# Kernel optimization log

Measured on AMD Instinct MI355X. Metric: run time of the kernel, lower is better.

## Reference

```python
import jax, jax.numpy as jnp
import numpy as np

N_USER = 100000
N_ITEM = 150000
N = N_USER + N_ITEM
D = 64            # latdim
NNZ = 1250000     # sparse adjacency nnz
BATCH = 16384     # node_ids batch
NUM_GNN_LAYERS = 2
GD = 16           # gate_dim (mamba d_model)
DSTATE = 8
DCONV = 4
EXPAND = 2
DINNER = GD * EXPAND  # 32
DTRANK = 1            # ceil(GD/16)
TEMP = 0.8            # gate_temp


def setup_inputs() -> dict:
    key = jax.random.key(0)
    ks = jax.random.split(key, 20)
    f32 = jnp.float32
    inp = {}
    inp["user_embedding"] = jax.random.normal(ks[0], (N_USER, D), f32) * 0.02
    inp["item_embedding"] = jax.random.normal(ks[1], (N_ITEM, D), f32) * 0.02
    inp["edge_row"] = jax.random.randint(ks[2], (NNZ,), 0, N, dtype=jnp.int32)
    inp["edge_col"] = jax.random.randint(ks[3], (NNZ,), 0, N, dtype=jnp.int32)
    inp["edge_val"] = jax.random.uniform(ks[4], (NNZ,), f32) * 0.1
    inp["node_ids"] = jax.random.randint(ks[5], (BATCH,), 0, N, dtype=jnp.int32)
    # gate params (torch Linear weight layout: [out, in])
    inp["down_w"] = jax.random.normal(ks[6], (GD, D), f32) * 0.02
    inp["in_proj_w"] = jax.random.normal(ks[7], (2 * DINNER, GD), f32) * 0.05
    inp["conv_w"] = jax.random.normal(ks[8], (DINNER, DCONV), f32) * 0.1
    inp["conv_b"] = jnp.zeros((DINNER,), f32)
    inp["x_proj_w"] = jax.random.normal(ks[9], (DTRANK + 2 * DSTATE, DINNER), f32) * 0.05
    inp["dt_proj_w"] = jax.random.normal(ks[10], (DINNER, DTRANK), f32) * 0.1
    inp["dt_proj_b"] = jax.random.normal(ks[11], (DINNER,), f32) * 0.1
    inp["A_log"] = jnp.log(jnp.broadcast_to(jnp.arange(1, DSTATE + 1, dtype=f32), (DINNER, DSTATE)))
    inp["D_param"] = jnp.ones((DINNER,), f32)
    inp["out_proj_w"] = jax.random.normal(ks[12], (GD, DINNER), f32) * 0.05
    inp["ln_g"] = jnp.ones((GD,), f32)
    inp["ln_b"] = jnp.zeros((GD,), f32)
    inp["to_logit_w"] = jax.random.normal(ks[13], (1, GD), f32) * 0.02
    inp["to_logit_b"] = jnp.zeros((1,), f32)
    return inp


def _mamba(g, in_proj_w, conv_w, conv_b, x_proj_w, dt_proj_w, dt_proj_b, A_log, D_param, out_proj_w):
    # g: [B, L, GD] -- standard Mamba block (selective scan)
    Bsz, L, _ = g.shape
    xz = g @ in_proj_w.T                     # [B,L,2*DINNER]
    x, z = jnp.split(xz, 2, axis=-1)         # each [B,L,DINNER]
    # causal depthwise conv1d along L (padding = DCONV-1, truncated to L)
    xp = jnp.pad(x, ((0, 0), (DCONV - 1, 0), (0, 0)))
    xconv = sum(xp[:, k:k + L, :] * conv_w[:, k] for k in range(DCONV)) + conv_b
    x = jax.nn.silu(xconv)
    dbc = x @ x_proj_w.T                     # [B,L,DTRANK+2*DSTATE]
    dt = dbc[..., :DTRANK]
    Bm = dbc[..., DTRANK:DTRANK + DSTATE]
    Cm = dbc[..., DTRANK + DSTATE:]
    dt = jax.nn.softplus(dt @ dt_proj_w.T + dt_proj_b)   # [B,L,DINNER]
    A = -jnp.exp(A_log)                                   # [DINNER,DSTATE]
    dA = jnp.exp(dt[..., None] * A)                       # [B,L,DINNER,DSTATE]
    dBx = dt[..., None] * Bm[:, :, None, :] * x[..., None]

    def step(h, ins):
        dA_t, dBx_t = ins
        h = dA_t * h + dBx_t
        return h, h

    h0 = jnp.zeros((Bsz, DINNER, DSTATE), x.dtype)
    _, hs = jax.lax.scan(step, h0, (jnp.swapaxes(dA, 0, 1), jnp.swapaxes(dBx, 0, 1)))
    hs = jnp.swapaxes(hs, 0, 1)                           # [B,L,DINNER,DSTATE]
    y = jnp.einsum('blds,bls->bld', hs, Cm) + D_param * x
    y = y * jax.nn.silu(z)
    return y @ out_proj_w.T                               # [B,L,GD]


def reference(user_embedding, item_embedding, edge_val, down_w, in_proj_w, conv_w,
              conv_b, x_proj_w, dt_proj_w, dt_proj_b, A_log, D_param, out_proj_w,
              ln_g, ln_b, to_logit_w, to_logit_b, edge_row, edge_col, node_ids):
    embeds = jnp.concatenate([user_embedding, item_embedding], axis=0)   # [N,D]
    seqs = [embeds[node_ids]]
    for _ in range(NUM_GNN_LAYERS):
        # sparse adjacency aggregation: out[r] += val * embeds[c]
        msg = edge_val[:, None] * embeds[edge_col]                       # [NNZ,D]
        embeds = jax.ops.segment_sum(msg, edge_row, num_segments=N)      # [N,D]
        # F.normalize(p=2, dim=1)
        nrm = jnp.linalg.norm(embeds, axis=1, keepdims=True)
        embeds = embeds / jnp.maximum(nrm, 1e-12)
        seqs.append(embeds[node_ids])
    seq = jnp.stack(seqs, axis=1)                                        # [B,L,D]

    # MambaDepthGating._compute_logits (deg_cond disabled)
    g = seq @ down_w.T                                                   # [B,L,GD]
    y = _mamba(g, in_proj_w, conv_w, conv_b, x_proj_w, dt_proj_w, dt_proj_b,
               A_log, D_param, out_proj_w)
    y = y + g
    mu = y.mean(-1, keepdims=True)
    var = y.var(-1, keepdims=True)
    y = (y - mu) / jnp.sqrt(var + 1e-12) * ln_g + ln_b                   # LN eps=1e-12
    logits = (y @ to_logit_w.T + to_logit_b)[..., 0]                     # [B,L]

    # fuse_from_logits, L=3 > 2 -> softmax path, perturbed=False
    w = jax.nn.softmax(logits / max(TEMP, 1e-6), axis=1)                 # [B,L]
    fused = jnp.sum(seq * w[..., None], axis=1)                          # [B,D]
    return fused
```

## Files before the change

kernel.cpp:

```cpp
#include <hip/hip_runtime.h>
#include <math.h>

#define N_USER 100000
#define N_ITEM 150000
#define NTOT   250000
#define D64    64
#define NNZ    1250000
#define BATCH  16384
#define GD     16
#define DSTATE 8
#define DCONV  4
#define DINNER 32
#define LSEQ   3
#define NBLK1  ((NTOT + 1023) >> 10)

__global__ void zero4_kernel(int4* __restrict__ p, int n4) {
    int i = blockIdx.x * blockDim.x + threadIdx.x;
    if (i < n4) p[i] = make_int4(0, 0, 0, 0);
}

__global__ void mark_nids_kernel(const int* __restrict__ nids,
                                 unsigned char* __restrict__ nidf,
                                 unsigned char* __restrict__ needf) {
    int b = blockIdx.x * 256 + threadIdx.x;
    if (b < BATCH) { int r = nids[b]; nidf[r] = 1; needf[r] = 1; }
}

__global__ void mark_need_kernel(const int* __restrict__ erow,
                                 const int* __restrict__ ecol,
                                 const unsigned char* __restrict__ nidf,
                                 unsigned char* __restrict__ needf) {
    int e = blockIdx.x * 256 + threadIdx.x;
    if (e < NNZ && nidf[erow[e]]) needf[ecol[e]] = 1;
}

__global__ void hist_slot_kernel(const int* __restrict__ erow,
                                 const unsigned char* __restrict__ needf,
                                 int* __restrict__ cnt, int* __restrict__ slot) {
    int e = blockIdx.x * 256 + threadIdx.x;
    if (e >= NNZ) return;
    int r = erow[e];
    if (needf[r]) slot[e] = atomicAdd(&cnt[r], 1);
}

__global__ __launch_bounds__(256) void scan1_kernel(const int* __restrict__ cnt,
                                                    int* __restrict__ offs,
                                                    int* __restrict__ bsum) {
    __shared__ int lds[256];
    int t = threadIdx.x;
    int base = (blockIdx.x << 10) + (t << 2);
    int d0 = (base + 0 < NTOT) ? cnt[base + 0] : 0;
    int d1 = (base + 1 < NTOT) ? cnt[base + 1] : 0;
    int d2 = (base + 2 < NTOT) ? cnt[base + 2] : 0;
    int d3 = (base + 3 < NTOT) ? cnt[base + 3] : 0;
    int s = d0 + d1 + d2 + d3;
    lds[t] = s;
    __syncthreads();
    for (int off = 1; off < 256; off <<= 1) {
        int v = (t >= off) ? lds[t - off] : 0;
        __syncthreads();
        lds[t] += v;
        __syncthreads();
    }
    int excl = lds[t] - s;
    if (base + 0 < NTOT) offs[base + 0] = excl;
    if (base + 1 < NTOT) offs[base + 1] = excl + d0;
    if (base + 2 < NTOT) offs[base + 2] = excl + d0 + d1;
    if (base + 3 < NTOT) offs[base + 3] = excl + d0 + d1 + d2;
    if (t == 255) bsum[blockIdx.x] = lds[255];
}

__global__ __launch_bounds__(256) void scan2_kernel(int* __restrict__ bsum) {
    __shared__ int lds[256];
    int t = threadIdx.x;
    int v0 = (t < NBLK1) ? bsum[t] : 0;
    lds[t] = v0;
    __syncthreads();
    for (int off = 1; off < 256; off <<= 1) {
        int v = (t >= off) ? lds[t - off] : 0;
        __syncthreads();
        lds[t] += v;
        __syncthreads();
    }
    if (t < NBLK1) bsum[t] = lds[t] - v0;
}

__global__ void scan3_kernel(int* __restrict__ offs, const int* __restrict__ bsum,
                             const int* __restrict__ cnt) {
    int i = blockIdx.x * 256 + threadIdx.x;
    if (i >= NTOT) return;
    int v = offs[i] + bsum[i >> 10];
    offs[i] = v;
    if (i == NTOT - 1) offs[NTOT] = v + cnt[i];
}

__global__ void fill_kernel(const int* __restrict__ erow, const int* __restrict__ ecol,
                            const float* __restrict__ eval_, const int* __restrict__ offs,
                            const int* __restrict__ slot,
                            const unsigned char* __restrict__ needf,
                            int2* __restrict__ colval) {
    int e = blockIdx.x * 256 + threadIdx.x;
    if (e >= NNZ) return;
    int r = erow[e];
    if (!needf[r]) return;
    colval[offs[r] + slot[e]] = make_int2(ecol[e], __float_as_int(eval_[e]));
}

__global__ __launch_bounds__(256) void layer1_kernel(const float* __restrict__ user,
                                                     const float* __restrict__ item,
                                                     const unsigned char* __restrict__ needf,
                                                     const int*  __restrict__ offs,
                                                     const int2* __restrict__ colval,
                                                     float* __restrict__ dst) {
    const float4* user4 = (const float4*)user;
    const float4* item4 = (const float4*)item;

    int row    = (blockIdx.x << 4) + (threadIdx.x >> 4);
    int lane16 = threadIdx.x & 15;
    if (row >= NTOT) return;
    if (!needf[row]) return;
    int o0 = offs[row], o1 = offs[row + 1];

    float4 acc = make_float4(0.f, 0.f, 0.f, 0.f);
    int i = o0;
    for (; i + 2 <= o1; i += 2) {
        int2 cv0 = colval[i];
        int2 cv1 = colval[i + 1];
        const float4* s0 = (cv0.x < N_USER) ? user4 + (size_t)cv0.x * 16
                                            : item4 + (size_t)(cv0.x - N_USER) * 16;
        const float4* s1 = (cv1.x < N_USER) ? user4 + (size_t)cv1.x * 16
                                            : item4 + (size_t)(cv1.x - N_USER) * 16;
        float4 v0 = s0[lane16];
        float4 v1 = s1[lane16];
        float w0 = __int_as_float(cv0.y);
        float w1 = __int_as_float(cv1.y);
        acc.x = fmaf(w1, v1.x, fmaf(w0, v0.x, acc.x));
        acc.y = fmaf(w1, v1.y, fmaf(w0, v0.y, acc.y));
        acc.z = fmaf(w1, v1.z, fmaf(w0, v0.z, acc.z));
        acc.w = fmaf(w1, v1.w, fmaf(w0, v0.w, acc.w));
    }
    if (i < o1) {
        int2 cv = colval[i];
        const float4* s0 = (cv.x < N_USER) ? user4 + (size_t)cv.x * 16
                                           : item4 + (size_t)(cv.x - N_USER) * 16;
        float4 v = s0[lane16];
        float w = __int_as_float(cv.y);
        acc.x = fmaf(w, v.x, acc.x);
        acc.y = fmaf(w, v.y, acc.y);
        acc.z = fmaf(w, v.z, acc.z);
        acc.w = fmaf(w, v.w, acc.w);
    }

    float s = fmaf(acc.x, acc.x, fmaf(acc.y, acc.y, fmaf(acc.z, acc.z, acc.w * acc.w)));
    #pragma unroll
    for (int m = 8; m >= 1; m >>= 1) s += __shfl_xor(s, m, 64);
    float scale = 1.f / fmaxf(sqrtf(s), 1e-12f);
    float4 r;
    r.x = acc.x * scale; r.y = acc.y * scale; r.z = acc.z * scale; r.w = acc.w * scale;
    ((float4*)dst)[(size_t)row * 16 + lane16] = r;
}

__global__ __launch_bounds__(256) void layer2_kernel(const float* __restrict__ embA,
                                                     const int*  __restrict__ nids,
                                                     const int*  __restrict__ offs,
                                                     const int2* __restrict__ colval,
                                                     float* __restrict__ embBc) {
    const float4* src4 = (const float4*)embA;
    int idx    = (blockIdx.x << 4) + (threadIdx.x >> 4);
    int lane16 = threadIdx.x & 15;
    if (idx >= BATCH) return;
    int row = nids[idx];
    int o0 = offs[row], o1 = offs[row + 1];

    float4 acc = make_float4(0.f, 0.f, 0.f, 0.f);
    int i = o0;
    for (; i + 2 <= o1; i += 2) {
        int2 cv0 = colval[i];
        int2 cv1 = colval[i + 1];
        float4 v0 = src4[(size_t)cv0.x * 16 + lane16];
        float4 v1 = src4[(size_t)cv1.x * 16 + lane16];
        float w0 = __int_as_float(cv0.y);
        float w1 = __int_as_float(cv1.y);
        acc.x = fmaf(w1, v1.x, fmaf(w0, v0.x, acc.x));
        acc.y = fmaf(w1, v1.y, fmaf(w0, v0.y, acc.y));
        acc.z = fmaf(w1, v1.z, fmaf(w0, v0.z, acc.z));
        acc.w = fmaf(w1, v1.w, fmaf(w0, v0.w, acc.w));
    }
    if (i < o1) {
        int2 cv = colval[i];
        float4 v = src4[(size_t)cv.x * 16 + lane16];
        float w = __int_as_float(cv.y);
        acc.x = fmaf(w, v.x, acc.x);
        acc.y = fmaf(w, v.y, acc.y);
        acc.z = fmaf(w, v.z, acc.z);
        acc.w = fmaf(w, v.w, acc.w);
    }

    float s = fmaf(acc.x, acc.x, fmaf(acc.y, acc.y, fmaf(acc.z, acc.z, acc.w * acc.w)));
    #pragma unroll
    for (int m = 8; m >= 1; m >>= 1) s += __shfl_xor(s, m, 64);
    float scale = 1.f / fmaxf(sqrtf(s), 1e-12f);
    float4 r;
    r.x = acc.x * scale; r.y = acc.y * scale; r.z = acc.z * scale; r.w = acc.w * scale;
    ((float4*)embBc)[(size_t)idx * 16 + lane16] = r;
}

__global__ __launch_bounds__(64, 1) void final_kernel(
    const int*   __restrict__ nids,
    const float* __restrict__ user,      const float* __restrict__ item,
    const float* __restrict__ embA,      const float* __restrict__ embBc,
    const float* __restrict__ down_w,    const float* __restrict__ in_proj_w,
    const float* __restrict__ conv_w,    const float* __restrict__ conv_b,
    const float* __restrict__ x_proj_w,  const float* __restrict__ dt_proj_w,
    const float* __restrict__ dt_proj_b, const float* __restrict__ A_log,
    const float* __restrict__ D_param,   const float* __restrict__ out_proj_w,
    const float* __restrict__ ln_g,      const float* __restrict__ ln_b,
    const float* __restrict__ to_logit_w,const float* __restrict__ to_logit_b,
    float* __restrict__ out) {

    __shared__ float4 s_down4[GD * 16];
    __shared__ float4 s_ipx4[DINNER * 4];
    __shared__ float4 s_ipz4[DINNER * 4];
    __shared__ float  s_xpT[DINNER * 17];
    __shared__ float4 s_cw4[DINNER];
    __shared__ float  s_cb[DINNER];
    __shared__ float  s_dtw[DINNER], s_dtb[DINNER], s_Dp[DINNER];
    __shared__ float  s_A[DINNER * DSTATE];
    __shared__ float4 s_opT4[DINNER * 4];
    __shared__ float  s_lng[GD], s_lnb[GD], s_lw[GD];
    __shared__ float  s_lb;

    int t = threadIdx.x;
    {
        const float4* dw4 = (const float4*)down_w;
        for (int i = t; i < GD * 16; i += 64) s_down4[i] = dw4[i];
        const float4* ip4 = (const float4*)in_proj_w;
        for (int i = t; i < DINNER * 4; i += 64) { s_ipx4[i] = ip4[i]; s_ipz4[i] = ip4[DINNER * 4 + i]; }
        for (int i = t; i < DINNER * 17; i += 64) {
            int d = i / 17, r = i % 17;
            s_xpT[i] = x_proj_w[r * DINNER + d];
        }
        const float4* cw4 = (const float4*)conv_w;
        for (int i = t; i < DINNER; i += 64) {
            s_cw4[i] = cw4[i]; s_cb[i] = conv_b[i]; s_dtw[i] = dt_proj_w[i];
            s_dtb[i] = dt_proj_b[i]; s_Dp[i] = D_param[i];
        }
        for (int i = t; i < DINNER * DSTATE; i += 64) s_A[i] = -expf(A_log[i]);
        float* s_opT = (float*)s_opT4;
        for (int i = t; i < DINNER * GD; i += 64) {
            int d = i >> 4, j = i & 15;
            s_opT[i] = out_proj_w[j * DINNER + d];
        }
        if (t < GD) { s_lng[t] = ln_g[t]; s_lnb[t] = ln_b[t]; s_lw[t] = to_logit_w[t]; }
        if (t == 0) s_lb = to_logit_b[0];
    }
    __syncthreads();

    int b = blockIdx.x * 64 + t;
    int nid = nids[b];
    const float4* p0 = (const float4*)((nid < N_USER) ? user + (size_t)nid * D64
                                                      : item + (size_t)(nid - N_USER) * D64);
    const float4* p1 = (const float4*)(embA + (size_t)nid * D64);
    const float4* p2 = (const float4*)(embBc + (size_t)b * D64);

    float g[LSEQ][GD];
    #pragma unroll
    for (int l = 0; l < LSEQ; ++l)
        #pragma unroll
        for (int j = 0; j < GD; ++j) g[l][j] = 0.f;
    #pragma unroll
    for (int q = 0; q < 16; ++q) {
        float4 v0 = p0[q], v1 = p1[q], v2 = p2[q];
        #pragma unroll
        for (int j = 0; j < GD; ++j) {
            float4 w = s_down4[j * 16 + q];
            g[0][j] = fmaf(v0.x, w.x, fmaf(v0.y, w.y, fmaf(v0.z, w.z, fmaf(v0.w, w.w, g[0][j]))));
            g[1][j] = fmaf(v1.x, w.x, fmaf(v1.y, w.y, fmaf(v1.z, w.z, fmaf(v1.w, w.w, g[1][j]))));
            g[2][j] = fmaf(v2.x, w.x, fmaf(v2.y, w.y, fmaf(v2.z, w.z, fmaf(v2.w, w.w, g[2][j]))));
        }
    }

    #define COMPUTE_XS(d, xs0, xs1, xs2)                                          \
        float xs0, xs1, xs2;                                                      \
        {                                                                         \
            float xl0 = 0.f, xl1 = 0.f, xl2 = 0.f;                                \
            _Pragma("unroll")                                                     \
            for (int qq = 0; qq < 4; ++qq) {                                      \
                float4 w = s_ipx4[(d) * 4 + qq];                                  \
                xl0 = fmaf(g[0][4*qq+0], w.x, fmaf(g[0][4*qq+1], w.y,             \
                      fmaf(g[0][4*qq+2], w.z, fmaf(g[0][4*qq+3], w.w, xl0))));    \
                xl1 = fmaf(g[1][4*qq+0], w.x, fmaf(g[1][4*qq+1], w.y,             \
                      fmaf(g[1][4*qq+2], w.z, fmaf(g[1][4*qq+3], w.w, xl1))));    \
                xl2 = fmaf(g[2][4*qq+0], w.x, fmaf(g[2][4*qq+1], w.y,             \
                      fmaf(g[2][4*qq+2], w.z, fmaf(g[2][4*qq+3], w.w, xl2))));    \
            }                                                                     \
            float4 cw = s_cw4[d]; float cb = s_cb[d];                             \
            float a0 = fmaf(xl0, cw.w, cb);                                       \
            float a1 = fmaf(xl1, cw.w, fmaf(xl0, cw.z, cb));                      \
            float a2 = fmaf(xl2, cw.w, fmaf(xl1, cw.z, fmaf(xl0, cw.y, cb)));     \
            xs0 = a0 / (1.f + __expf(-a0));                                       \
            xs1 = a1 / (1.f + __expf(-a1));                                       \
            xs2 = a2 / (1.f + __expf(-a2));                                       \
        }

    float dtr[LSEQ] = {0.f, 0.f, 0.f};
    float Bm[LSEQ][DSTATE], Cm[LSEQ][DSTATE];
    #pragma unroll
    for (int l = 0; l < LSEQ; ++l)
        #pragma unroll
        for (int s = 0; s < DSTATE; ++s) { Bm[l][s] = 0.f; Cm[l][s] = 0.f; }

    for (int d = 0; d < DINNER; ++d) {
        COMPUTE_XS(d, xs0, xs1, xs2)
        const float* xt = s_xpT + d * 17;
        float w = xt[0];
        dtr[0] = fmaf(xs0, w, dtr[0]); dtr[1] = fmaf(xs1, w, dtr[1]); dtr[2] = fmaf(xs2, w, dtr[2]);
        #pragma unroll
        for (int s = 0; s < DSTATE; ++s) {
            float wb = xt[1 + s], wc = xt[9 + s];
            Bm[0][s] = fmaf(xs0, wb, Bm[0][s]); Bm[1][s] = fmaf(xs1, wb, Bm[1][s]); Bm[2][s] = fmaf(xs2, wb, Bm[2][s]);
            Cm[0][s] = fmaf(xs0, wc, Cm[0][s]); Cm[1][s] = fmaf(xs1, wc, Cm[1][s]); Cm[2][s] = fmaf(xs2, wc, Cm[2][s]);
        }
    }

    float o[LSEQ][GD];
    #pragma unroll
    for (int l = 0; l < LSEQ; ++l)
        #pragma unroll
        for (int j = 0; j < GD; ++j) o[l][j] = 0.f;

    for (int d = 0; d < DINNER; ++d) {
        COMPUTE_XS(d, ys0, ys1, ys2)
        float xsv[3] = {ys0, ys1, ys2};
        float As[DSTATE];
        #pragma unroll
        for (int s = 0; s < DSTATE; ++s) As[s] = s_A[d * DSTATE + s];
        float dtw = s_dtw[d], dtb = s_dtb[d], Dp = s_Dp[d];
        float h[DSTATE];
        #pragma unroll
        for (int s = 0; s < DSTATE; ++s) h[s] = 0.f;
        #pragma unroll
        for (int l = 0; l < LSEQ; ++l) {
            float pre = fmaf(dtr[l], dtw, dtb);
            float dt  = (pre > 20.f) ? pre : __logf(1.f + __expf(pre));
            float xv  = xsv[l];
            float dtx = dt * xv;
            float acc = 0.f;
            #pragma unroll
            for (int s = 0; s < DSTATE; ++s) {
                float dA = __expf(dt * As[s]);
                h[s] = fmaf(dA, h[s], dtx * Bm[l][s]);
                acc  = fmaf(h[s], Cm[l][s], acc);
            }
            float y = fmaf(Dp, xv, acc);
            float zv = 0.f;
            #pragma unroll
            for (int qq = 0; qq < 4; ++qq) {
                float4 w = s_ipz4[d * 4 + qq];
                zv = fmaf(g[l][4*qq+0], w.x, fmaf(g[l][4*qq+1], w.y,
                     fmaf(g[l][4*qq+2], w.z, fmaf(g[l][4*qq+3], w.w, zv))));
            }
            float ys = y * (zv / (1.f + __expf(-zv)));
            #pragma unroll
            for (int qq = 0; qq < 4; ++qq) {
                float4 w = s_opT4[d * 4 + qq];
                o[l][4*qq+0] = fmaf(ys, w.x, o[l][4*qq+0]);
                o[l][4*qq+1] = fmaf(ys, w.y, o[l][4*qq+1]);
                o[l][4*qq+2] = fmaf(ys, w.z, o[l][4*qq+2]);
                o[l][4*qq+3] = fmaf(ys, w.w, o[l][4*qq+3]);
            }
        }
    }

    float lg[LSEQ];
    #pragma unroll
    for (int l = 0; l < LSEQ; ++l) {
        float mu = 0.f;
        #pragma unroll
        for (int j = 0; j < GD; ++j) { o[l][j] += g[l][j]; mu += o[l][j]; }
        mu *= (1.f / GD);
        float var = 0.f;
        #pragma unroll
        for (int j = 0; j < GD; ++j) { float dd = o[l][j] - mu; var = fmaf(dd, dd, var); }
        var *= (1.f / GD);
        float inv = rsqrtf(var + 1e-12f);
        float lo = 0.f;
        #pragma unroll
        for (int j = 0; j < GD; ++j)
            lo = fmaf(fmaf((o[l][j] - mu) * inv, s_lng[j], s_lnb[j]), s_lw[j], lo);
        lg[l] = (lo + s_lb) * (1.0f / 0.8f);
    }
    float mx = fmaxf(lg[0], fmaxf(lg[1], lg[2]));
    float e0 = __expf(lg[0] - mx), e1 = __expf(lg[1] - mx), e2 = __expf(lg[2] - mx);
    float inv = 1.f / (e0 + e1 + e2);
    float w0 = e0 * inv, w1 = e1 * inv, w2 = e2 * inv;

    float4* o4 = (float4*)(out + (size_t)b * D64);
    #pragma unroll
    for (int q = 0; q < 16; ++q) {
        float4 a = p0[q], bb = p1[q], c = p2[q], r;
        r.x = w0 * a.x + w1 * bb.x + w2 * c.x;
        r.y = w0 * a.y + w1 * bb.y + w2 * c.y;
        r.z = w0 * a.z + w1 * bb.z + w2 * c.z;
        r.w = w0 * a.w + w1 * bb.w + w2 * c.w;
        o4[q] = r;
    }
}

extern "C" void kernel_launch(void* const* d_in, const int* in_sizes, int n_in,
                              void* d_out, int out_size, void* d_ws, size_t ws_size,
                              hipStream_t stream) {
    const float* user      = (const float*)d_in[0];
    const float* item      = (const float*)d_in[1];
    const int*   erow      = (const int*)  d_in[2];
    const int*   ecol      = (const int*)  d_in[3];
    const float* eval_     = (const float*)d_in[4];
    const int*   nids      = (const int*)  d_in[5];
    const float* down_w    = (const float*)d_in[6];
    const float* in_proj_w = (const float*)d_in[7];
    const float* conv_w    = (const float*)d_in[8];
    const float* conv_b    = (const float*)d_in[9];
    const float* x_proj_w  = (const float*)d_in[10];
    const float* dt_proj_w = (const float*)d_in[11];
    const float* dt_proj_b = (const float*)d_in[12];
    const float* A_log     = (const float*)d_in[13];
    const float* D_param   = (const float*)d_in[14];
    const float* out_projw = (const float*)d_in[15];
    const float* ln_g      = (const float*)d_in[16];
    const float* ln_b      = (const float*)d_in[17];
    const float* to_lw     = (const float*)d_in[18];
    const float* to_lb     = (const float*)d_in[19];
    float* out = (float*)d_out;

    char* base = (char*)d_ws;
    float* embA  = (float*)base;
    float* embBc = (float*)(base + 64000000);
    char* c = base + 64000000 + 4194304;
    int* cnt = (int*)c;
    unsigned char* nidf  = (unsigned char*)(c + 1000000);
    unsigned char* needf = (unsigned char*)(c + 1250000);
    c += 1500032;
    int* offs = (int*)c;  c += (size_t)(NTOT + 1) * 4 + 60;
    int* bsum = (int*)c;  c += 1024;
    int* slot = (int*)c;  c += (size_t)NNZ * 4;
    int2* colval = (int2*)c;

    zero4_kernel<<<(1500032 / 16 + 255) / 256, 256, 0, stream>>>((int4*)cnt, 1500032 / 16);
    mark_nids_kernel<<<(BATCH + 255) / 256, 256, 0, stream>>>(nids, nidf, needf);
    mark_need_kernel<<<(NNZ + 255) / 256, 256, 0, stream>>>(erow, ecol, nidf, needf);

    hist_slot_kernel<<<(NNZ + 255) / 256, 256, 0, stream>>>(erow, needf, cnt, slot);
    scan1_kernel<<<NBLK1, 256, 0, stream>>>(cnt, offs, bsum);
    scan2_kernel<<<1, 256, 0, stream>>>(bsum);
    scan3_kernel<<<(NTOT + 255) / 256, 256, 0, stream>>>(offs, bsum, cnt);
    fill_kernel<<<(NNZ + 255) / 256, 256, 0, stream>>>(erow, ecol, eval_, offs, slot, needf, colval);

    layer1_kernel<<<NTOT / 16, 256, 0, stream>>>(user, item, needf, offs, colval, embA);
    layer2_kernel<<<BATCH / 16, 256, 0, stream>>>(embA, nids, offs, colval, embBc);

    final_kernel<<<BATCH / 64, 64, 0, stream>>>(nids, user, item, embA, embBc,
                                                down_w, in_proj_w, conv_w, conv_b,
                                                x_proj_w, dt_proj_w, dt_proj_b, A_log,
                                                D_param, out_projw, ln_g, ln_b, to_lw, to_lb, out);
}
```

Measured before the change: 291.0 us.

## Parallelize final gating kernel across 16 lanes per batch element via shared memory

Rewrites the Mamba gating/fusion kernel so each batch element is handled by 16 cooperating lanes instead of one thread. Rows are loaded coalesced into shared memory, and the projections, scan and layer norm are split across lanes with shuffle reductions. This removes the heavy per-thread register arrays and the low-occupancy one-wave-per-block launch. In exchange it adds several block barriers and shared-memory staging. Variance now uses the E[x^2]-mu^2 form, which changes numerics slightly.

Measured after the change: 266.2 us. -8.5%, faster.

```diff
diff --git a/kernel.cpp b/kernel.cpp
--- a/kernel.cpp
+++ b/kernel.cpp
@@ -205,7 +205,7 @@
     ((float4*)embBc)[(size_t)idx * 16 + lane16] = r;
 }
 
-__global__ __launch_bounds__(64, 1) void final_kernel(
+__global__ __launch_bounds__(256) void final_kernel(
     const int*   __restrict__ nids,
     const float* __restrict__ user,      const float* __restrict__ item,
     const float* __restrict__ embA,      const float* __restrict__ embBc,
@@ -218,192 +218,214 @@
     const float* __restrict__ to_logit_w,const float* __restrict__ to_logit_b,
     float* __restrict__ out) {
 
-    __shared__ float4 s_down4[GD * 16];
-    __shared__ float4 s_ipx4[DINNER * 4];
-    __shared__ float4 s_ipz4[DINNER * 4];
+    __shared__ float4 s_rows4[16 * 49];
+    __shared__ float  s_downT[D64 * GD];
+    __shared__ float  s_ipxT[GD * DINNER];
+    __shared__ float  s_ipzT[GD * DINNER];
     __shared__ float  s_xpT[DINNER * 17];
+    __shared__ float  s_opT[DINNER * GD];
+    __shared__ float  s_AT[DSTATE * DINNER];
     __shared__ float4 s_cw4[DINNER];
-    __shared__ float  s_cb[DINNER];
-    __shared__ float  s_dtw[DINNER], s_dtb[DINNER], s_Dp[DINNER];
-    __shared__ float  s_A[DINNER * DSTATE];
-    __shared__ float4 s_opT4[DINNER * 4];
+    __shared__ float  s_cb[DINNER], s_dtw[DINNER], s_dtb[DINNER], s_Dp[DINNER];
     __shared__ float  s_lng[GD], s_lnb[GD], s_lw[GD];
     __shared__ float  s_lb;
+    __shared__ float  s_g[16 * 49];
+    __shared__ float  s_xs[16 * 98];
+    __shared__ float  s_dbc[16 * 49];
 
     int t = threadIdx.x;
-    {
-        const float4* dw4 = (const float4*)down_w;
-        for (int i = t; i < GD * 16; i += 64) s_down4[i] = dw4[i];
-        const float4* ip4 = (const float4*)in_proj_w;
-        for (int i = t; i < DINNER * 4; i += 64) { s_ipx4[i] = ip4[i]; s_ipz4[i] = ip4[DINNER * 4 + i]; }
-        for (int i = t; i < DINNER * 17; i += 64) {
-            int d = i / 17, r = i % 17;
-            s_xpT[i] = x_proj_w[r * DINNER + d];
+
+    for (int i = t; i < D64 * GD; i += 256) {
+        int j = i & 15, d = i >> 4;
+        s_downT[i] = down_w[j * D64 + d];
+    }
+    for (int i = t; i < GD * DINNER; i += 256) {
+        int d = i & 31, j = i >> 5;
+        s_ipxT[i] = in_proj_w[d * GD + j];
+        s_ipzT[i] = in_proj_w[(d + DINNER) * GD + j];
+    }
+    for (int i = t; i < DINNER * 17; i += 256) {
+        int d = i / 17, r = i % 17;
+        s_xpT[i] = x_proj_w[r * DINNER + d];
+    }
+    for (int i = t; i < DINNER * GD; i += 256) {
+        int j = i & 15, d = i >> 4;
+        s_opT[i] = out_proj_w[j * DINNER + d];
+    }
+    for (int i = t; i < DSTATE * DINNER; i += 256) {
+        int d = i & 31, s = i >> 5;
+        s_AT[i] = -expf(A_log[d * DSTATE + s]);
+    }
+    if (t < DINNER) {
+        s_cw4[t] = ((const float4*)conv_w)[t];
+        s_cb[t] = conv_b[t]; s_dtw[t] = dt_proj_w[t];
+        s_dtb[t] = dt_proj_b[t]; s_Dp[t] = D_param[t];
+    }
+    if (t < GD) { s_lng[t] = ln_g[t]; s_lnb[t] = ln_b[t]; s_lw[t] = to_logit_w[t]; }
+    if (t == 0) s_lb = to_logit_b[0];
+
+    int wave = t >> 6, lane = t & 63;
+    int grp = lane >> 4, lane16 = lane & 15;
+    int eb = wave * 4 + grp;
+    int b  = blockIdx.x * 16 + eb;
+    {
+        int nid = nids[b];
+        const float4* p0 = (const float4*)((nid < N_USER) ? user + (size_t)nid * D64
+                                                          : item + (size_t)(nid - N_USER) * D64);
+        const float4* p1 = (const float4*)(embA + (size_t)nid * D64);
+        const float4* p2 = (const float4*)(embBc + (size_t)b * D64);
+        s_rows4[eb * 49 + 0 * 16 + lane16] = p0[lane16];
+        s_rows4[eb * 49 + 1 * 16 + lane16] = p1[lane16];
+        s_rows4[eb * 49 + 2 * 16 + lane16] = p2[lane16];
+    }
+    __syncthreads();
+
+    const float* rows = (const float*)s_rows4 + eb * 196;
+
+    {
+        float a0 = 0.f, a1 = 0.f, a2 = 0.f;
+        #pragma unroll
+        for (int d = 0; d < D64; ++d) {
+            float w = s_downT[d * GD + lane16];
+            a0 = fmaf(rows[d], w, a0);
+            a1 = fmaf(rows[64 + d], w, a1);
+            a2 = fmaf(rows[128 + d], w, a2);
         }
-        const float4* cw4 = (const float4*)conv_w;
-        for (int i = t; i < DINNER; i += 64) {
-            s_cw4[i] = cw4[i]; s_cb[i] = conv_b[i]; s_dtw[i] = dt_proj_w[i];
-            s_dtb[i] = dt_proj_b[i]; s_Dp[i] = D_param[i];
+        s_g[eb * 49 + 0 * GD + lane16] = a0;
+        s_g[eb * 49 + 1 * GD + lane16] = a1;
+        s_g[eb * 49 + 2 * GD + lane16] = a2;
+    }
+    __syncthreads();
+
+    const float* ge = s_g + eb * 49;
+
+    float xsr[2][LSEQ];
+    #pragma unroll
+    for (int c = 0; c < 2; ++c) {
+        int d = lane16 + 16 * c;
+        float xl0 = 0.f, xl1 = 0.f, xl2 = 0.f;
+        #pragma unroll
+        for (int j = 0; j < GD; ++j) {
+            float w = s_ipxT[j * DINNER + d];
+            xl0 = fmaf(ge[j], w, xl0);
+            xl1 = fmaf(ge[GD + j], w, xl1);
+            xl2 = fmaf(ge[2 * GD + j], w, xl2);
         }
-        for (int i = t; i < DINNER * DSTATE; i += 64) s_A[i] = -expf(A_log[i]);
-        float* s_opT = (float*)s_opT4;
-        for (int i = t; i < DINNER * GD; i += 64) {
-            int d = i >> 4, j = i & 15;
-            s_opT[i] = out_proj_w[j * DINNER + d];
+        float4 cw = s_cw4[d]; float cb = s_cb[d];
+        float a0 = fmaf(xl0, cw.w, cb);
+        float a1 = fmaf(xl1, cw.w, fmaf(xl0, cw.z, cb));
+        float a2 = fmaf(xl2, cw.w, fmaf(xl1, cw.z, fmaf(xl0, cw.y, cb)));
+        xsr[c][0] = a0 / (1.f + __expf(-a0));
+        xsr[c][1] = a1 / (1.f + __expf(-a1));
+        xsr[c][2] = a2 / (1.f + __expf(-a2));
+        #pragma unroll
+        for (int l = 0; l < LSEQ; ++l) s_xs[eb * 98 + l * DINNER + d] = xsr[c][l];
+    }
+    __syncthreads();
+
+    {
+        const float* xse = s_xs + eb * 98;
+        int nr = (lane16 == 0) ? 2 : 1;
+        for (int it = 0; it < nr; ++it) {
+            int r = (it == 0) ? lane16 : 16;
+            float a0 = 0.f, a1 = 0.f, a2 = 0.f;
+            #pragma unroll
+            for (int d = 0; d < DINNER; ++d) {
+                float w = s_xpT[d * 17 + r];
+                a0 = fmaf(xse[d], w, a0);
+                a1 = fmaf(xse[DINNER + d], w, a1);
+                a2 = fmaf(xse[2 * DINNER + d], w, a2);
+            }
+            s_dbc[eb * 49 + 0 * 17 + r] = a0;
+            s_dbc[eb * 49 + 1 * 17 + r] = a1;
+            s_dbc[eb * 49 + 2 * 17 + r] = a2;
         }
-        if (t < GD) { s_lng[t] = ln_g[t]; s_lnb[t] = ln_b[t]; s_lw[t] = to_logit_w[t]; }
-        if (t == 0) s_lb = to_logit_b[0];
-    }
-    __syncthreads();
-
-    int b = blockIdx.x * 64 + t;
-    int nid = nids[b];
-    const float4* p0 = (const float4*)((nid < N_USER) ? user + (size_t)nid * D64
-                                                      : item + (size_t)(nid - N_USER) * D64);
-    const float4* p1 = (const float4*)(embA + (size_t)nid * D64);
-    const float4* p2 = (const float4*)(embBc + (size_t)b * D64);
-
-    float g[LSEQ][GD];
-    #pragma unroll
-    for (int l = 0; l < LSEQ; ++l)
-        #pragma unroll
-        for (int j = 0; j < GD; ++j) g[l][j] = 0.f;
-    #pragma unroll
-    for (int q = 0; q < 16; ++q) {
-        float4 v0 = p0[q], v1 = p1[q], v2 = p2[q];
-        #pragma unroll
-        for (int j = 0; j < GD; ++j) {
-            float4 w = s_down4[j * 16 + q];
-            g[0][j] = fmaf(v0.x, w.x, fmaf(v0.y, w.y, fmaf(v0.z, w.z, fmaf(v0.w, w.w, g[0][j]))));
-            g[1][j] = fmaf(v1.x, w.x, fmaf(v1.y, w.y, fmaf(v1.z, w.z, fmaf(v1.w, w.w, g[1][j]))));
-            g[2][j] = fmaf(v2.x, w.x, fmaf(v2.y, w.y, fmaf(v2.z, w.z, fmaf(v2.w, w.w, g[2][j]))));
-        }
-    }
-
-    #define COMPUTE_XS(d, xs0, xs1, xs2)                                          \
-        float xs0, xs1, xs2;                                                      \
-        {                                                                         \
-            float xl0 = 0.f, xl1 = 0.f, xl2 = 0.f;                                \
-            _Pragma("unroll")                                                     \
-            for (int qq = 0; qq < 4; ++qq) {                                      \
-                float4 w = s_ipx4[(d) * 4 + qq];                                  \
-                xl0 = fmaf(g[0][4*qq+0], w.x, fmaf(g[0][4*qq+1], w.y,             \
-                      fmaf(g[0][4*qq+2], w.z, fmaf(g[0][4*qq+3], w.w, xl0))));    \
-                xl1 = fmaf(g[1][4*qq+0], w.x, fmaf(g[1][4*qq+1], w.y,             \
-                      fmaf(g[1][4*qq+2], w.z, fmaf(g[1][4*qq+3], w.w, xl1))));    \
-                xl2 = fmaf(g[2][4*qq+0], w.x, fmaf(g[2][4*qq+1], w.y,             \
-                      fmaf(g[2][4*qq+2], w.z, fmaf(g[2][4*qq+3], w.w, xl2))));    \
-            }                                                                     \
-            float4 cw = s_cw4[d]; float cb = s_cb[d];                             \
-            float a0 = fmaf(xl0, cw.w, cb);                                       \
-            float a1 = fmaf(xl1, cw.w, fmaf(xl0, cw.z, cb));                      \
-            float a2 = fmaf(xl2, cw.w, fmaf(xl1, cw.z, fmaf(xl0, cw.y, cb)));     \
-            xs0 = a0 / (1.f + __expf(-a0));                                       \
-            xs1 = a1 / (1.f + __expf(-a1));                                       \
-            xs2 = a2 / (1.f + __expf(-a2));                                       \
-        }
-
-    float dtr[LSEQ] = {0.f, 0.f, 0.f};
-    float Bm[LSEQ][DSTATE], Cm[LSEQ][DSTATE];
-    #pragma unroll
-    for (int l = 0; l < LSEQ; ++l)
-        #pragma unroll
-        for (int s = 0; s < DSTATE; ++s) { Bm[l][s] = 0.f; Cm[l][s] = 0.f; }
-
-    for (int d = 0; d < DINNER; ++d) {
-        COMPUTE_XS(d, xs0, xs1, xs2)
-        const float* xt = s_xpT + d * 17;
-        float w = xt[0];
-        dtr[0] = fmaf(xs0, w, dtr[0]); dtr[1] = fmaf(xs1, w, dtr[1]); dtr[2] = fmaf(xs2, w, dtr[2]);
-        #pragma unroll
-        for (int s = 0; s < DSTATE; ++s) {
-            float wb = xt[1 + s], wc = xt[9 + s];
-            Bm[0][s] = fmaf(xs0, wb, Bm[0][s]); Bm[1][s] = fmaf(xs1, wb, Bm[1][s]); Bm[2][s] = fmaf(xs2, wb, Bm[2][s]);
-            Cm[0][s] = fmaf(xs0, wc, Cm[0][s]); Cm[1][s] = fmaf(xs1, wc, Cm[1][s]); Cm[2][s] = fmaf(xs2, wc, Cm[2][s]);
-        }
-    }
-
-    float o[LSEQ][GD];
-    #pragma unroll
-    for (int l = 0; l < LSEQ; ++l)
-        #pragma unroll
-        for (int j = 0; j < GD; ++j) o[l][j] = 0.f;
-
-    for (int d = 0; d < DINNER; ++d) {
-        COMPUTE_XS(d, ys0, ys1, ys2)
-        float xsv[3] = {ys0, ys1, ys2};
-        float As[DSTATE];
-        #pragma unroll
-        for (int s = 0; s < DSTATE; ++s) As[s] = s_A[d * DSTATE + s];
-        float dtw = s_dtw[d], dtb = s_dtb[d], Dp = s_Dp[d];
-        float h[DSTATE];
-        #pragma unroll
-        for (int s = 0; s < DSTATE; ++s) h[s] = 0.f;
+    }
+    __syncthreads();
+
+    {
+        const float* dbce = s_dbc + eb * 49;
+        float h[2][DSTATE];
+        #pragma unroll
+        for (int c = 0; c < 2; ++c)
+            #pragma unroll
+            for (int s = 0; s < DSTATE; ++s) h[c][s] = 0.f;
         #pragma unroll
         for (int l = 0; l < LSEQ; ++l) {
-            float pre = fmaf(dtr[l], dtw, dtb);
-            float dt  = (pre > 20.f) ? pre : __logf(1.f + __expf(pre));
-            float xv  = xsv[l];
-            float dtx = dt * xv;
-            float acc = 0.f;
+            float dtr = dbce[l * 17];
+            float Bm[DSTATE], Cm[DSTATE];
             #pragma unroll
             for (int s = 0; s < DSTATE; ++s) {
-                float dA = __expf(dt * As[s]);
-                h[s] = fmaf(dA, h[s], dtx * Bm[l][s]);
-                acc  = fmaf(h[s], Cm[l][s], acc);
+                Bm[s] = dbce[l * 17 + 1 + s];
+                Cm[s] = dbce[l * 17 + 9 + s];
             }
-            float y = fmaf(Dp, xv, acc);
-            float zv = 0.f;
-            #pragma unroll
-            for (int qq = 0; qq < 4; ++qq) {
-                float4 w = s_ipz4[d * 4 + qq];
-                zv = fmaf(g[l][4*qq+0], w.x, fmaf(g[l][4*qq+1], w.y,
-                     fmaf(g[l][4*qq+2], w.z, fmaf(g[l][4*qq+3], w.w, zv))));
-            }
-            float ys = y * (zv / (1.f + __expf(-zv)));
-            #pragma unroll
-            for (int qq = 0; qq < 4; ++qq) {
-                float4 w = s_opT4[d * 4 + qq];
-                o[l][4*qq+0] = fmaf(ys, w.x, o[l][4*qq+0]);
-                o[l][4*qq+1] = fmaf(ys, w.y, o[l][4*qq+1]);
-                o[l][4*qq+2] = fmaf(ys, w.z, o[l][4*qq+2]);
-                o[l][4*qq+3] = fmaf(ys, w.w, o[l][4*qq+3]);
+            #pragma unroll
+            for (int c = 0; c < 2; ++c) {
+                int d = lane16 + 16 * c;
+                float pre = fmaf(dtr, s_dtw[d], s_dtb[d]);
+                float dt  = (pre > 20.f) ? pre : __logf(1.f + __expf(pre));
+                float xv  = xsr[c][l];
+                float dtx = dt * xv;
+                float acc = 0.f;
+                #pragma unroll
+                for (int s = 0; s < DSTATE; ++s) {
+                    float dA = __expf(dt * s_AT[s * DINNER + d]);
+                    h[c][s] = fmaf(dA, h[c][s], dtx * Bm[s]);
+                    acc = fmaf(h[c][s], Cm[s], acc);
+                }
+                float y = fmaf(s_Dp[d], xv, acc);
+                float zv = 0.f;
+                #pragma unroll
+                for (int j = 0; j < GD; ++j)
+                    zv = fmaf(ge[l * GD + j], s_ipzT[j * DINNER + d], zv);
+                float ys = y * (zv / (1.f + __expf(-zv)));
+                s_xs[eb * 98 + l * DINNER + d] = ys;
             }
         }
     }
+    __syncthreads();
 
     float lg[LSEQ];
-    #pragma unroll
-    for (int l = 0; l < LSEQ; ++l) {
-        float mu = 0.f;
-        #pragma unroll
-        for (int j = 0; j < GD; ++j) { o[l][j] += g[l][j]; mu += o[l][j]; }
-        mu *= (1.f / GD);
-        float var = 0.f;
-        #pragma unroll
-        for (int j = 0; j < GD; ++j) { float dd = o[l][j] - mu; var = fmaf(dd, dd, var); }
-        var *= (1.f / GD);
-        float inv = rsqrtf(var + 1e-12f);
-        float lo = 0.f;
-        #pragma unroll
-        for (int j = 0; j < GD; ++j)
-            lo = fmaf(fmaf((o[l][j] - mu) * inv, s_lng[j], s_lnb[j]), s_lw[j], lo);
-        lg[l] = (lo + s_lb) * (1.0f / 0.8f);
-    }
-    float mx = fmaxf(lg[0], fmaxf(lg[1], lg[2]));
-    float e0 = __expf(lg[0] - mx), e1 = __expf(lg[1] - mx), e2 = __expf(lg[2] - mx);
-    float inv = 1.f / (e0 + e1 + e2);
-    float w0 = e0 * inv, w1 = e1 * inv, w2 = e2 * inv;
-
-    float4* o4 = (float4*)(out + (size_t)b * D64);
-    #pragma unroll
-    for (int q = 0; q < 16; ++q) {
-        float4 a = p0[q], bb = p1[q], c = p2[q], r;
-        r.x = w0 * a.x + w1 * bb.x + w2 * c.x;
-        r.y = w0 * a.y + w1 * bb.y + w2 * c.y;
-        r.z = w0 * a.z + w1 * bb.z + w2 * c.z;
-        r.w = w0 * a.w + w1 * bb.w + w2 * c.w;
-        o4[q] = r;
+    {
+        const float* yse = s_xs + eb * 98;
+        #pragma unroll
+        for (int l = 0; l < LSEQ; ++l) {
+            float a = 0.f;
+            #pragma unroll
+            for (int d = 0; d < DINNER; ++d)
+                a = fmaf(yse[l * DINNER + d], s_opT[d * GD + lane16], a);
+            float v = a + ge[l * GD + lane16];
+            float sm = v, sq = v * v;
+            #pragma unroll
+            for (int m = 1; m <= 8; m <<= 1) {
+                sm += __shfl_xor(sm, m, 64);
+                sq += __shfl_xor(sq, m, 64);
+            }
+            float mu  = sm * (1.f / GD);
+            float var = fmaxf(sq * (1.f / GD) - mu * mu, 0.f);
+            float inv = rsqrtf(var + 1e-12f);
+            float lo = fmaf(fmaf((v - mu) * inv, s_lng[lane16], s_lnb[lane16]),
+                            s_lw[lane16], 0.f);
+            #pragma unroll
+            for (int m = 1; m <= 8; m <<= 1) lo += __shfl_xor(lo, m, 64);
+            lg[l] = (lo + s_lb) * 1.25f;
+        }
+    }
+
+    {
+        float mx = fmaxf(lg[0], fmaxf(lg[1], lg[2]));
+        float e0 = __expf(lg[0] - mx), e1 = __expf(lg[1] - mx), e2 = __expf(lg[2] - mx);
+        float inv = 1.f / (e0 + e1 + e2);
+        float w0 = e0 * inv, w1 = e1 * inv, w2 = e2 * inv;
+        float4 r0 = s_rows4[eb * 49 + 0 * 16 + lane16];
+        float4 r1 = s_rows4[eb * 49 + 1 * 16 + lane16];
+        float4 r2 = s_rows4[eb * 49 + 2 * 16 + lane16];
+        float4 r;
+        r.x = w0 * r0.x + w1 * r1.x + w2 * r2.x;
+        r.y = w0 * r0.y + w1 * r1.y + w2 * r2.y;
+        r.z = w0 * r0.z + w1 * r1.z + w2 * r2.z;
+        r.w = w0 * r0.w + w1 * r1.w + w2 * r2.w;
+        ((float4*)out)[(size_t)b * 16 + lane16] = r;
     }
 }
 
@@ -458,8 +480,8 @@
     layer1_kernel<<<NTOT / 16, 256, 0, stream>>>(user, item, needf, offs, colval, embA);
     layer2_kernel<<<BATCH / 16, 256, 0, stream>>>(embA, nids, offs, colval, embBc);
 
-    final_kernel<<<BATCH / 64, 64, 0, stream>>>(nids, user, item, embA, embBc,
-                                                down_w, in_proj_w, conv_w, conv_b,
-                                                x_proj_w, dt_proj_w, dt_proj_b, A_log,
-                                                D_param, out_projw, ln_g, ln_b, to_lw, to_lb, out);
-}
+    final_kernel<<<BATCH / 16, 256, 0, stream>>>(nids, user, item, embA, embBc,
+                                                 down_w, in_proj_w, conv_w, conv_b,
+                                                 x_proj_w, dt_proj_w, dt_proj_b, A_log,
+                                                 D_param, out_projw, ln_g, ln_b, to_lw, to_lb, out);
+}
```
